# Kernel tuning notes

Measured on AMD Instinct MI355X. Metric: run time of the kernel, lower is better.

Reference implementation:

```python
import jax, jax.numpy as jnp
import numpy as np

WINDOW_SIZE, SM, PS = 8, 2, 2  # window_size, spatial_merge_size, patch_size
SMU = SM * SM  # spatial_merge_unit


def _window_index(grid_thw):
    """Numpy port of get_window_index; returns permutation of arange(S)."""
    vmws = WINDOW_SIZE // SM // PS  # 2
    out, wid = [], 0
    for t, h, w in grid_thw:
        lh, lw = h // SM, w // SM
        idx = np.arange(t * lh * lw).reshape(t, lh, lw)
        ph = vmws - lh % vmws
        pw = vmws - lw % vmws
        nh, nw = (lh + ph) // vmws, (lw + pw) // vmws
        pad = np.full((t, lh + ph, lw + pw), -100, dtype=np.int64)
        pad[:, :lh, :lw] = idx
        pad = pad.reshape(t, nh, vmws, nw, vmws).transpose(0, 1, 3, 2, 4).reshape(-1)
        out.append(pad[pad != -100] + wid)
        wid += t * lh * lw
    return np.concatenate(out).astype(np.int32)


def setup_inputs() -> dict:
    key = jax.random.key(0)
    ks = jax.random.split(key, 5)
    B, T, C, H = 1, 16384, 1280, 16
    D = C // H  # 80
    grid_thw = np.array([[1, 256, 256]], dtype=np.int64)  # llm grid 128x128 -> S=16384
    wi = _window_index(grid_thw)
    x = jax.random.normal(ks[0], (B, T, C), jnp.float32)
    cos = jax.random.normal(ks[1], (B * T, 1, D), jnp.float32)
    sin = jax.random.normal(ks[2], (B * T, 1, D), jnp.float32)
    W_qkv = jax.random.normal(ks[3], (C, 3 * C), jnp.float32) * (C ** -0.5)
    W_proj = jax.random.normal(ks[4], (C, C), jnp.float32) * (C ** -0.5)
    # each window: (vmws*vmws) merged tokens * SMU patches = 16 tokens
    block_size = (WINDOW_SIZE // SM // PS) ** 2 * SMU
    return {"x": x, "cos": cos, "sin": sin, "W_qkv": W_qkv, "W_proj": W_proj,
            "window_index": jnp.asarray(wi), "block_size": block_size}


def reference(x, cos, sin, W_qkv, W_proj, window_index, block_size):
    B, T, C = x.shape
    S = B * T
    D = cos.shape[-1]
    H = C // D
    # window reorder (gather)
    xr = x.reshape(S, C)[window_index]
    qkv = (xr @ W_qkv).reshape(S, 3, H, D)
    q, k, v = qkv[:, 0], qkv[:, 1], qkv[:, 2]
    # module's (unusual) q/k mixing 'rotary'
    cw, sw = cos[window_index], sin[window_index]  # (S,1,D) broadcast over heads
    qr = q * cw + k * sw
    kr = k * cw - q * sw
    # block-diagonal attention: uniform 16-token windows -> reshape, no SxS mask
    nb = S // block_size
    qb = qr.reshape(nb, block_size, H, D)
    kb = kr.reshape(nb, block_size, H, D)
    vb = v.reshape(nb, block_size, H, D)
    att = jnp.einsum('bqhd,bkhd->bhqk', qb, kb) * (D ** -0.5)
    att = jax.nn.softmax(att, axis=-1)
    y = jnp.einsum('bhqk,bkhd->bqhd', att, vb).reshape(S, C)
    # undo window reorder
    y = y[jnp.argsort(window_index)]
    return y.reshape(B, T, C) @ W_proj
```

## Files before the change

kernel.cpp:

```cpp
#include <hip/hip_runtime.h>
#include <hip/hip_bf16.h>

#define S_TOK   16384
#define C_DIM   1280
#define C3_DIM  3840
#define H_DIM   16
#define D_DIM   80
#define BLK     16
#define PLANE_ELEMS ((size_t)S_TOK * C_DIM)

using u16x8  = __attribute__((ext_vector_type(8))) unsigned short;
using u16x4  = __attribute__((ext_vector_type(4))) unsigned short;
using bf16x8 = __attribute__((ext_vector_type(8))) __bf16;
using f32x4  = __attribute__((ext_vector_type(4))) float;

__device__ __forceinline__ unsigned short f2bf(float f) {
    return __bfloat16_as_ushort(__float2bfloat16(f));
}
__device__ __forceinline__ float bf2f(unsigned short u) {
    unsigned int x = (unsigned int)u << 16;
    return __builtin_bit_cast(float, x);
}
__device__ __forceinline__ void gload_lds16(const unsigned short* g, unsigned short* l) {
    __builtin_amdgcn_global_load_lds(
        (const __attribute__((address_space(1))) void*)g,
        (__attribute__((address_space(3))) void*)l, 16, 0, 0);
}
__device__ __forceinline__ bf16x8 lds_read_swz(const unsigned short* buf,
                                               int off, int xr, int cb) {
    return *(const bf16x8*)((const char*)buf + off + (cb ^ xr));
}

__global__ __launch_bounds__(256) void transpose_cvt(
    const float* __restrict__ W, unsigned short* __restrict__ WT, int K, int N)
{
    __shared__ float tile[32][33];
    const int n0 = blockIdx.x * 32, k0 = blockIdx.y * 32;
    const int tx = threadIdx.x & 31, ty = threadIdx.x >> 5;
#pragma unroll
    for (int i = ty; i < 32; i += 8)
        tile[i][tx] = W[(size_t)(k0 + i) * N + n0 + tx];
    __syncthreads();
#pragma unroll
    for (int i = ty; i < 32; i += 8)
        WT[(size_t)(n0 + i) * K + k0 + tx] = f2bf(tile[tx][i]);
}

__global__ __launch_bounds__(256) void gather_cvt(
    const float* __restrict__ x, const int* __restrict__ wi,
    unsigned short* __restrict__ xg)
{
    int idx = blockIdx.x * 256 + threadIdx.x;
    int s  = idx / 160;
    int c8 = (idx - s * 160) * 8;
    const float* src = x + (size_t)wi[s] * C_DIM + c8;
    f32x4 v0 = *(const f32x4*)src;
    f32x4 v1 = *(const f32x4*)(src + 4);
    u16x8 o;
    o[0]=f2bf(v0[0]); o[1]=f2bf(v0[1]); o[2]=f2bf(v0[2]); o[3]=f2bf(v0[3]);
    o[4]=f2bf(v1[0]); o[5]=f2bf(v1[1]); o[6]=f2bf(v1[2]); o[7]=f2bf(v1[3]);
    *(u16x8*)&xg[(size_t)s * C_DIM + c8] = o;
}

__global__ __launch_bounds__(256) void inv_perm(
    const int* __restrict__ wi, int* __restrict__ inv)
{
    int s = blockIdx.x * 256 + threadIdx.x;
    inv[wi[s]] = s;
}

#define BK2 64

template<int OUTMODE, bool GATHER>
__global__ __launch_bounds__(512, 2) void gemm256(
    const unsigned short* __restrict__ A,
    const unsigned short* __restrict__ BT,
    void* __restrict__ Cp,
    const int* __restrict__ row_map,
    int N, int K)
{
    __shared__ __align__(16) unsigned short AsB[2 * 16384];
    __shared__ __align__(16) unsigned short BsB[2 * 16384];

    const int m0   = blockIdx.x * 256;
    const int n0   = blockIdx.y * 256;
    const int tid  = threadIdx.x;
    const int lane = tid & 63;
    const int wv   = tid >> 6;
    const int wm   = (wv >> 2) * 128;
    const int wn   = (wv & 3) * 64;
    const int lrow = lane & 15;
    const int quad = lane >> 4;

    const unsigned short* pa[4];
    const unsigned short* pb[4];
#pragma unroll
    for (int i = 0; i < 4; i++) {
        int gch = i * 512 + tid;
        int r   = gch >> 3;
        int c   = ((gch & 7) ^ (r & 7)) << 3;
        int ga  = GATHER ? row_map[m0 + r] : (m0 + r);
        pa[i] = A  + (size_t)ga * K + c;
        pb[i] = BT + (size_t)(n0 + r) * K + c;
    }

    int aoff[8], axr[8], boff[4], bxr[4];
#pragma unroll
    for (int mt = 0; mt < 8; mt++) {
        int r = wm + mt * 16 + lrow;
        aoff[mt] = r << 7;  axr[mt] = (r & 7) << 4;
    }
#pragma unroll
    for (int nt = 0; nt < 4; nt++) {
        int r = wn + nt * 16 + lrow;
        boff[nt] = r << 7;  bxr[nt] = (r & 7) << 4;
    }

    f32x4 acc[8][4];
#pragma unroll
    for (int i = 0; i < 8; i++)
#pragma unroll
        for (int j = 0; j < 4; j++)
            acc[i][j] = (f32x4){0.f, 0.f, 0.f, 0.f};

    const int NT = K >> 6;

    auto stage = [&](int bsel, int koff) {
#pragma unroll
        for (int i = 0; i < 4; i++)
            gload_lds16(pa[i] + koff, AsB + bsel * 16384 + i * 4096 + wv * 512);
#pragma unroll
        for (int i = 0; i < 4; i++)
            gload_lds16(pb[i] + koff, BsB + bsel * 16384 + i * 4096 + wv * 512);
    };

    stage(0, 0);
    stage(1, BK2);
    asm volatile("s_waitcnt vmcnt(8)" ::: "memory");
    __builtin_amdgcn_sched_barrier(0);
    __builtin_amdgcn_s_barrier();
    __builtin_amdgcn_sched_barrier(0);

    int cur = 0;
    for (int t = 0; t < NT; ++t) {
        const unsigned short* Ac = AsB + cur * 16384;
        const unsigned short* Bc = BsB + cur * 16384;
        const int cb0 = quad << 4;
        const int cb1 = 64 + (quad << 4);

        bf16x8 a0[8], b0[4];
#pragma unroll
        for (int mt = 0; mt < 8; mt++) a0[mt] = lds_read_swz(Ac, aoff[mt], axr[mt], cb0);
#pragma unroll
        for (int nt = 0; nt < 4; nt++) b0[nt] = lds_read_swz(Bc, boff[nt], bxr[nt], cb0);
        __builtin_amdgcn_s_setprio(1);
#pragma unroll
        for (int mt = 0; mt < 8; mt++)
#pragma unroll
            for (int nt = 0; nt < 4; nt++)
                acc[mt][nt] = __builtin_amdgcn_mfma_f32_16x16x32_bf16(
                    a0[mt], b0[nt], acc[mt][nt], 0, 0, 0);
        __builtin_amdgcn_s_setprio(0);

        bf16x8 a1[8], b1[4];
#pragma unroll
        for (int mt = 0; mt < 8; mt++) a1[mt] = lds_read_swz(Ac, aoff[mt], axr[mt], cb1);
#pragma unroll
        for (int nt = 0; nt < 4; nt++) b1[nt] = lds_read_swz(Bc, boff[nt], bxr[nt], cb1);
        __builtin_amdgcn_s_setprio(1);
#pragma unroll
        for (int mt = 0; mt < 4; mt++)
#pragma unroll
            for (int nt = 0; nt < 4; nt++)
                acc[mt][nt] = __builtin_amdgcn_mfma_f32_16x16x32_bf16(
                    a1[mt], b1[nt], acc[mt][nt], 0, 0, 0);
        __builtin_amdgcn_s_setprio(0);
        asm volatile("s_waitcnt lgkmcnt(0)" ::: "memory");
        __builtin_amdgcn_sched_barrier(0);
        __builtin_amdgcn_s_barrier();
        __builtin_amdgcn_sched_barrier(0);

        if (t + 2 < NT) stage(cur, (t + 2) * BK2);
        __builtin_amdgcn_s_setprio(1);
#pragma unroll
        for (int mt = 4; mt < 8; mt++)
#pragma unroll
            for (int nt = 0; nt < 4; nt++)
                acc[mt][nt] = __builtin_amdgcn_mfma_f32_16x16x32_bf16(
                    a1[mt], b1[nt], acc[mt][nt], 0, 0, 0);
        __builtin_amdgcn_s_setprio(0);
        if (t + 2 < NT) {
            asm volatile("s_waitcnt vmcnt(8)" ::: "memory");
        } else if (t + 1 < NT) {
            asm volatile("s_waitcnt vmcnt(0)" ::: "memory");
        }
        __builtin_amdgcn_sched_barrier(0);
        __builtin_amdgcn_s_barrier();
        __builtin_amdgcn_sched_barrier(0);
        cur ^= 1;
    }

#pragma unroll
    for (int nt = 0; nt < 4; nt++) {
        const int cb = n0 + wn + nt * 16;
        unsigned short* pp = nullptr;
        if (OUTMODE == 2) {
            int which = cb / C_DIM;
            int hc    = cb - which * C_DIM;
            int h     = hc / D_DIM;
            int d0    = hc - h * D_DIM;
            pp = (unsigned short*)Cp + (size_t)which * PLANE_ELEMS
               + (size_t)h * S_TOK * D_DIM + d0 + lrow;
        }
#pragma unroll
        for (int mt = 0; mt < 8; mt++)
#pragma unroll
            for (int r = 0; r < 4; r++) {
                int row = m0 + wm + mt * 16 + quad * 4 + r;
                if (OUTMODE == 0)
                    ((float*)Cp)[(size_t)row * N + cb + lrow] = acc[mt][nt][r];
                else
                    pp[(size_t)row * D_DIM] = f2bf(acc[mt][nt][r]);
            }
    }
}

__global__ __launch_bounds__(256) void attn_v2(
    const unsigned short* __restrict__ planes,
    const float* __restrict__ cosp,
    const float* __restrict__ sinp,
    const int* __restrict__ wi,
    unsigned short* __restrict__ yw)
{
    __shared__ __align__(16) unsigned short Q_lds[4][16][88];
    __shared__ __align__(16) unsigned short K_lds[4][16][88];
    __shared__ __align__(16) unsigned short V_lds[4][1536];

    const int wave = threadIdx.x >> 6;
    const int lane = threadIdx.x & 63;
    const int b    = blockIdx.y;
    const int h    = blockIdx.x * 4 + wave;
    const int j16  = lane & 15;
    const int quad = lane >> 4;

    const unsigned short* Vsrc = planes + 2 * PLANE_ELEMS
        + ((size_t)h * S_TOK + b * BLK) * D_DIM;
    unsigned short* Vsl = &V_lds[wave][0];
#pragma unroll
    for (int c = 0; c < 3; c++)
        gload_lds16(Vsrc + c * 512 + lane * 8, Vsl + c * 512);

    const unsigned short* Qbase = planes + ((size_t)h * S_TOK + b * BLK) * D_DIM;
#pragma unroll
    for (int c = 0; c < 3; c++) {
        int ch = c * 64 + lane;
        if (ch < 160) {
            int r  = ch / 10;
            int d8 = (ch - r * 10) * 8;
            int crow = wi[b * BLK + r];
            const unsigned short* Qp = Qbase + (size_t)r * D_DIM + d8;
            u16x8 qv = *(const u16x8*)Qp;
            u16x8 kv = *(const u16x8*)(Qp + PLANE_ELEMS);
            const float* cp = cosp + (size_t)crow * D_DIM + d8;
            const float* sp = sinp + (size_t)crow * D_DIM + d8;
            f32x4 c0 = *(const f32x4*)cp, c1 = *(const f32x4*)(cp + 4);
            f32x4 s0 = *(const f32x4*)sp, s1 = *(const f32x4*)(sp + 4);
            u16x8 qo, ko;
#pragma unroll
            for (int j = 0; j < 8; j++) {
                float cw = (j < 4) ? c0[j] : c1[j - 4];
                float sw = (j < 4) ? s0[j] : s1[j - 4];
                float q = bf2f(qv[j]), k = bf2f(kv[j]);
                qo[j] = f2bf(q * cw + k * sw);
                ko[j] = f2bf(k * cw - q * sw);
            }
            *(u16x8*)&Q_lds[wave][r][d8] = qo;
            *(u16x8*)&K_lds[wave][r][d8] = ko;
        }
    }

    asm volatile("s_waitcnt vmcnt(0)" ::: "memory");
    __builtin_amdgcn_sched_barrier(0);

    const u16x8 zz = {0, 0, 0, 0, 0, 0, 0, 0};
    bf16x8 qf[3], kf[3];
#pragma unroll
    for (int s = 0; s < 3; s++) {
        int dcol = 32 * s + quad * 8;
        bool pad = (dcol >= D_DIM);
        int dc = pad ? 0 : dcol;
        u16x8 qv = *(const u16x8*)&Q_lds[wave][j16][dc];
        u16x8 kv = *(const u16x8*)&K_lds[wave][j16][dc];
        if (pad) { qv = zz; kv = zz; }
        qf[s] = __builtin_bit_cast(bf16x8, qv);
        kf[s] = __builtin_bit_cast(bf16x8, kv);
    }

    f32x4 sacc = (f32x4){0.f, 0.f, 0.f, 0.f};
#pragma unroll
    for (int s = 0; s < 3; s++)
        sacc = __builtin_amdgcn_mfma_f32_16x16x32_bf16(kf[s], qf[s], sacc, 0, 0, 0);

    const float scale = 0.11180339887498948f;
    float sc[4];
#pragma unroll
    for (int r = 0; r < 4; r++) sc[r] = sacc[r] * scale;
    float m = fmaxf(fmaxf(sc[0], sc[1]), fmaxf(sc[2], sc[3]));
    m = fmaxf(m, __shfl_xor(m, 16));
    m = fmaxf(m, __shfl_xor(m, 32));
    float e[4], sum = 0.f;
#pragma unroll
    for (int r = 0; r < 4; r++) { e[r] = __expf(sc[r] - m); sum += e[r]; }
    sum += __shfl_xor(sum, 16);
    sum += __shfl_xor(sum, 32);
    float inv = 1.f / sum;

    int sl = quad * 32 + j16;
    float pv0[4], pv1[4];
#pragma unroll
    for (int r = 0; r < 4; r++) pv0[r] = __shfl(e[r], sl & 63);
#pragma unroll
    for (int r = 0; r < 4; r++) pv1[r] = __shfl(e[r], (sl + 16) & 63);
    u16x8 pf;
#pragma unroll
    for (int r = 0; r < 4; r++) {
        pf[r]     = (quad < 2) ? f2bf(pv0[r]) : (unsigned short)0;
        pf[r + 4] = (quad < 2) ? f2bf(pv1[r]) : (unsigned short)0;
    }
    bf16x8 pfrag = __builtin_bit_cast(bf16x8, pf);

    u16x8 vf[5];
#pragma unroll
    for (int t = 0; t < 5; t++) {
#pragma unroll
        for (int e8 = 0; e8 < 8; e8++) {
            int kks = quad * 8 + e8;
            if (kks >= BLK) kks = e8;
            vf[t][e8] = Vsl[kks * D_DIM + t * 16 + j16];
        }
    }

    unsigned short* yrow = yw + (size_t)(b * BLK + j16) * C_DIM
                         + h * D_DIM + quad * 4;
#pragma unroll
    for (int t = 0; t < 5; t++) {
        f32x4 o = __builtin_amdgcn_mfma_f32_16x16x32_bf16(
            __builtin_bit_cast(bf16x8, vf[t]), pfrag,
            (f32x4){0.f, 0.f, 0.f, 0.f}, 0, 0, 0);
        u16x4 ov;
#pragma unroll
        for (int r = 0; r < 4; r++) ov[r] = f2bf(o[r] * inv);
        *(u16x4*)(yrow + t * 16) = ov;
    }
}

extern "C" void kernel_launch(void* const* d_in, const int* in_sizes, int n_in,
                              void* d_out, int out_size, void* d_ws, size_t ws_size,
                              hipStream_t stream)
{
    const float* x     = (const float*)d_in[0];
    const float* cosp  = (const float*)d_in[1];
    const float* sinp  = (const float*)d_in[2];
    const float* Wqkv  = (const float*)d_in[3];
    const float* Wproj = (const float*)d_in[4];
    const int*   wi    = (const int*)d_in[5];

    char* ws = (char*)d_ws;
    unsigned short* planes = (unsigned short*)ws;
    unsigned short* yw     = (unsigned short*)(ws + 125829120ull);
    unsigned short* wqkvT  = (unsigned short*)(ws + 167772160ull);
    unsigned short* wprojT = (unsigned short*)(ws + 177602560ull);
    unsigned short* xg     = (unsigned short*)(ws + 180879360ull);
    int*            inv    = (int*)(ws + 180879360ull);

    transpose_cvt<<<dim3(C3_DIM / 32, C_DIM / 32), 256, 0, stream>>>(
        Wqkv, wqkvT, C_DIM, C3_DIM);
    transpose_cvt<<<dim3(C_DIM / 32, C_DIM / 32), 256, 0, stream>>>(
        Wproj, wprojT, C_DIM, C_DIM);

    gather_cvt<<<S_TOK * 160 / 256, 256, 0, stream>>>(x, wi, xg);

    gemm256<2, false><<<dim3(S_TOK / 256, C3_DIM / 256), 512, 0, stream>>>(
        xg, wqkvT, planes, nullptr, C3_DIM, C_DIM);

    inv_perm<<<S_TOK / 256, 256, 0, stream>>>(wi, inv);

    attn_v2<<<dim3(H_DIM / 4, S_TOK / BLK), 256, 0, stream>>>(
        planes, cosp, sinp, wi, yw);

    gemm256<0, true><<<dim3(S_TOK / 256, C_DIM / 256), 512, 0, stream>>>(
        yw, wprojT, d_out, inv, C_DIM, C_DIM);
}
```

Before: 508.7 us.

## Swizzle GEMM block order, simplify main-loop schedule, use 128x128 GEMM for projection

Remaps the 256x256 GEMM's workgroup IDs with an XCD-aware swizzle so that neighbouring tiles share the L2 of one chiplet. It also merges the split second MFMA phase into a single loop and issues the next prefetch after the barrier. The output projection moves to a new simpler 128x128-tile GEMM with 256 threads and no double buffering, which gives more workgroups for the small N=1280 problem. The trade is that the new kernel has no software pipelining, and the reordered schedule may overlap loads and MFMAs less well.

```diff
diff --git a/kernel.cpp b/kernel.cpp
--- a/kernel.cpp
+++ b/kernel.cpp
@@ -82,8 +82,13 @@
     __shared__ __align__(16) unsigned short AsB[2 * 16384];
     __shared__ __align__(16) unsigned short BsB[2 * 16384];
 
-    const int m0   = blockIdx.x * 256;
-    const int n0   = blockIdx.y * 256;
+    const int nwg  = gridDim.x * gridDim.y;
+    const int wgid = blockIdx.y * gridDim.x + blockIdx.x;
+    const int cpx  = nwg >> 3;
+    const int swz  = (wgid & 7) * cpx + (wgid >> 3);
+    const int m0   = (swz % gridDim.x) * 256;
+    const int n0   = (swz / gridDim.x) * 256;
+
     const int tid  = threadIdx.x;
     const int lane = tid & 63;
     const int wv   = tid >> 6;
@@ -153,6 +158,7 @@
         for (int mt = 0; mt < 8; mt++) a0[mt] = lds_read_swz(Ac, aoff[mt], axr[mt], cb0);
 #pragma unroll
         for (int nt = 0; nt < 4; nt++) b0[nt] = lds_read_swz(Bc, boff[nt], bxr[nt], cb0);
+
         __builtin_amdgcn_s_setprio(1);
 #pragma unroll
         for (int mt = 0; mt < 8; mt++)
@@ -160,36 +166,27 @@
             for (int nt = 0; nt < 4; nt++)
                 acc[mt][nt] = __builtin_amdgcn_mfma_f32_16x16x32_bf16(
                     a0[mt], b0[nt], acc[mt][nt], 0, 0, 0);
-        __builtin_amdgcn_s_setprio(0);
 
         bf16x8 a1[8], b1[4];
 #pragma unroll
         for (int mt = 0; mt < 8; mt++) a1[mt] = lds_read_swz(Ac, aoff[mt], axr[mt], cb1);
 #pragma unroll
         for (int nt = 0; nt < 4; nt++) b1[nt] = lds_read_swz(Bc, boff[nt], bxr[nt], cb1);
-        __builtin_amdgcn_s_setprio(1);
-#pragma unroll
-        for (int mt = 0; mt < 4; mt++)
+#pragma unroll
+        for (int mt = 0; mt < 8; mt++)
 #pragma unroll
             for (int nt = 0; nt < 4; nt++)
                 acc[mt][nt] = __builtin_amdgcn_mfma_f32_16x16x32_bf16(
                     a1[mt], b1[nt], acc[mt][nt], 0, 0, 0);
         __builtin_amdgcn_s_setprio(0);
+
         asm volatile("s_waitcnt lgkmcnt(0)" ::: "memory");
         __builtin_amdgcn_sched_barrier(0);
         __builtin_amdgcn_s_barrier();
         __builtin_amdgcn_sched_barrier(0);
 
-        if (t + 2 < NT) stage(cur, (t + 2) * BK2);
-        __builtin_amdgcn_s_setprio(1);
-#pragma unroll
-        for (int mt = 4; mt < 8; mt++)
-#pragma unroll
-            for (int nt = 0; nt < 4; nt++)
-                acc[mt][nt] = __builtin_amdgcn_mfma_f32_16x16x32_bf16(
-                    a1[mt], b1[nt], acc[mt][nt], 0, 0, 0);
-        __builtin_amdgcn_s_setprio(0);
         if (t + 2 < NT) {
+            stage(cur, (t + 2) * BK2);
             asm volatile("s_waitcnt vmcnt(8)" ::: "memory");
         } else if (t + 1 < NT) {
             asm volatile("s_waitcnt vmcnt(0)" ::: "memory");
@@ -214,6 +211,115 @@
         }
 #pragma unroll
         for (int mt = 0; mt < 8; mt++)
+#pragma unroll
+            for (int r = 0; r < 4; r++) {
+                int row = m0 + wm + mt * 16 + quad * 4 + r;
+                if (OUTMODE == 0)
+                    ((float*)Cp)[(size_t)row * N + cb + lrow] = acc[mt][nt][r];
+                else
+                    pp[(size_t)row * D_DIM] = f2bf(acc[mt][nt][r]);
+            }
+    }
+}
+
+#define TM 128
+#define TN 128
+#define BK 64
+
+template<int OUTMODE, bool GATHER>
+__global__ __launch_bounds__(256) void gemm_mfma(
+    const unsigned short* __restrict__ A,
+    const unsigned short* __restrict__ BT,
+    void* __restrict__ Cp,
+    const int* __restrict__ row_map,
+    int N, int K)
+{
+    __shared__ __align__(16) unsigned short As[TM * BK];
+    __shared__ __align__(16) unsigned short Bs[TN * BK];
+
+    const int m0   = blockIdx.x * TM;
+    const int n0   = blockIdx.y * TN;
+    const int tid  = threadIdx.x;
+    const int lane = tid & 63;
+    const int wv   = tid >> 6;
+    const int wm   = (wv >> 1) * 64;
+    const int wn   = (wv & 1) * 64;
+    const int lrow = lane & 15;
+    const int quad = lane >> 4;
+
+    int gr[4], nr[4], csw[4];
+#pragma unroll
+    for (int c = 0; c < 4; c++) {
+        int ch = (wv * 4 + c) * 64 + lane;
+        int r  = ch >> 3;
+        csw[c] = ((ch & 7) ^ (r & 7)) << 3;
+        gr[c]  = GATHER ? row_map[m0 + r] : (m0 + r);
+        nr[c]  = n0 + r;
+    }
+
+    int aoff[4], asw[4], boff[4], bsw[4];
+#pragma unroll
+    for (int t = 0; t < 4; t++) {
+        int ra = wm + t * 16 + lrow;
+        aoff[t] = ra << 7;  asw[t] = (ra & 7) << 4;
+        int rb = wn + t * 16 + lrow;
+        boff[t] = rb << 7;  bsw[t] = (rb & 7) << 4;
+    }
+
+    f32x4 acc[4][4];
+#pragma unroll
+    for (int i = 0; i < 4; i++)
+#pragma unroll
+        for (int j = 0; j < 4; j++)
+            acc[i][j] = (f32x4){0.f, 0.f, 0.f, 0.f};
+
+    for (int kt = 0; kt < K; kt += BK) {
+#pragma unroll
+        for (int c = 0; c < 4; c++)
+            gload_lds16(A + (size_t)gr[c] * K + kt + csw[c],
+                        As + (wv * 4 + c) * 512);
+#pragma unroll
+        for (int c = 0; c < 4; c++)
+            gload_lds16(BT + (size_t)nr[c] * K + kt + csw[c],
+                        Bs + (wv * 4 + c) * 512);
+        __syncthreads();
+
+#pragma unroll
+        for (int ks = 0; ks < BK; ks += 32) {
+            const int cb = (ks << 1) + (quad << 4);
+            bf16x8 af[4], bfr[4];
+#pragma unroll
+            for (int mt = 0; mt < 4; mt++)
+                af[mt] = *(const bf16x8*)((const char*)As +
+                                          aoff[mt] + (cb ^ asw[mt]));
+#pragma unroll
+            for (int nt = 0; nt < 4; nt++)
+                bfr[nt] = *(const bf16x8*)((const char*)Bs +
+                                           boff[nt] + (cb ^ bsw[nt]));
+#pragma unroll
+            for (int mt = 0; mt < 4; mt++)
+#pragma unroll
+                for (int nt = 0; nt < 4; nt++)
+                    acc[mt][nt] = __builtin_amdgcn_mfma_f32_16x16x32_bf16(
+                        af[mt], bfr[nt], acc[mt][nt], 0, 0, 0);
+        }
+        __syncthreads();
+    }
+
+#pragma unroll
+    for (int nt = 0; nt < 4; nt++) {
+        const int cb = n0 + wn + nt * 16;
+        unsigned short* pp = nullptr;
+        if (OUTMODE == 2) {
+            int which = cb / C_DIM;
+            int hc    = cb - which * C_DIM;
+            int h     = hc / D_DIM;
+            int d0    = hc - h * D_DIM;
+            pp = (unsigned short*)Cp + (size_t)which * PLANE_ELEMS
+               + (size_t)h * S_TOK * D_DIM + d0 + lrow;
+        }
+#pragma unroll
+        for (int mt = 0; mt < 4; mt++)
 #pragma unroll
             for (int r = 0; r < 4; r++) {
                 int row = m0 + wm + mt * 16 + quad * 4 + r;
@@ -388,6 +494,6 @@
     attn_v2<<<dim3(H_DIM / 4, S_TOK / BLK), 256, 0, stream>>>(
         planes, cosp, sinp, wi, yw);
 
-    gemm256<0, true><<<dim3(S_TOK / 256, C_DIM / 256), 512, 0, stream>>>(
+    gemm_mfma<0, true><<<dim3(S_TOK / TM, C_DIM / TN), 256, 0, stream>>>(
         yw, wprojT, d_out, inv, C_DIM, C_DIM);
 }
```

New measurement: 494.9 us. 2.7% less time.
